# Performance work log

Hardware: AMD Instinct MI355X
Metric: run time of the kernel (lower is better)

## Reference

```python
import jax, jax.numpy as jnp
import numpy as np

B, S, H = 2, 2048, 2048
NH, NKV, D = 32, 8, 64
N_REP = NH // NKV  # 4
THETA = 10000.0


def _rotate_half(x):
    x1, x2 = jnp.split(x, 2, axis=-1)
    return jnp.concatenate([-x2, x1], axis=-1)


def _apply_rope(q, k, position_ids):
    # q: [B,NH,S,D], k: [B,NKV,S,D], position_ids: [B,S]
    inv_freq = 1.0 / (THETA ** (jnp.arange(0, D, 2, dtype=jnp.float32) / D))  # [D/2]
    ang = position_ids[:, None, :, None].astype(jnp.float32) * inv_freq      # [B,1,S,D/2]
    cos = jnp.concatenate([jnp.cos(ang), jnp.cos(ang)], axis=-1)             # [B,1,S,D]
    sin = jnp.concatenate([jnp.sin(ang), jnp.sin(ang)], axis=-1)
    q = q * cos + _rotate_half(q) * sin
    k = k * cos + _rotate_half(k) * sin
    return q, k


def setup_inputs() -> dict:
    key = jax.random.key(0)
    k1, k2, k3, k4 = jax.random.split(key, 4)
    hidden_states = jax.random.normal(k1, (B, S, H), dtype=jnp.float32)
    position_ids = jnp.broadcast_to(jnp.arange(S, dtype=jnp.int64 if jax.config.jax_enable_x64 else jnp.int32)[None, :], (B, S))
    Wq = jax.random.normal(k2, (H, NH * D), dtype=jnp.float32) * 0.02
    Wkv = jax.random.normal(k3, (H, NKV * 2 * D), dtype=jnp.float32) * 0.02
    Wo = jax.random.normal(k4, (H, H), dtype=jnp.float32) * 0.02
    return {"hidden_states": hidden_states, "position_ids": position_ids,
            "Wq": Wq, "Wkv": Wkv, "Wo": Wo}


def reference(hidden_states, position_ids, Wq, Wkv, Wo):
    b, s, _ = hidden_states.shape
    # fused QKV projections (Linear, no bias)
    q = (hidden_states @ Wq).reshape(b, s, NH, D).transpose(0, 2, 1, 3)      # [B,NH,S,D]
    kv = (hidden_states @ Wkv).reshape(b, s, NKV, 2, D)
    k = kv[:, :, :, 0, :].transpose(0, 2, 1, 3)                              # [B,NKV,S,D]
    v = kv[:, :, :, 1, :].transpose(0, 2, 1, 3)                              # [B,NKV,S,D]
    # rotary embedding
    q, k = _apply_rope(q, k, position_ids)
    # GQA: repeat_interleave K/V heads
    k = jnp.repeat(k, N_REP, axis=1)                                         # [B,NH,S,D]
    v = jnp.repeat(v, N_REP, axis=1)
    # causal SDPA (eval mode: dropout_p = 0)
    scale = 1.0 / np.sqrt(D)
    scores = jnp.einsum('bhqd,bhkd->bhqk', q, k) * scale                     # [B,NH,S,S]
    causal = jnp.tril(jnp.ones((s, s), dtype=bool))
    scores = jnp.where(causal[None, None], scores, jnp.finfo(scores.dtype).min)
    probs = jax.nn.softmax(scores, axis=-1)
    ctx = jnp.einsum('bhqk,bhkd->bhqd', probs, v)                            # [B,NH,S,D]
    ctx = ctx.transpose(0, 2, 1, 3).reshape(b, s, H)
    return ctx @ Wo
```

## Files before the change

### kernel.cpp

```cpp
#include <hip/hip_runtime.h>

typedef __bf16 bf16_t;
typedef __bf16 bf16x8 __attribute__((ext_vector_type(8)));
typedef __bf16 bf16x4 __attribute__((ext_vector_type(4)));
typedef float f32x4 __attribute__((ext_vector_type(4)));

#define DEV static __device__ __forceinline__

DEV void gload16(const void* g, void* lds) {
  __builtin_amdgcn_global_load_lds((__attribute__((address_space(1))) void*)g,
                                   (__attribute__((address_space(3))) void*)lds, 16, 0, 0);
}

DEV f32x4 mfma16(bf16x8 a, bf16x8 b, f32x4 c) {
  return __builtin_amdgcn_mfma_f32_16x16x32_bf16(a, b, c, 0, 0, 0);
}

DEV void transpose_blk(const float* __restrict__ in, bf16_t* __restrict__ out,
                       int R, int C, int bx, int by, int tid, float (*tile)[33]) {
  const int tx = tid & 31, ty = tid >> 5;
  const int rb = by * 32, cb = bx * 32;
#pragma unroll
  for (int i = 0; i < 32; i += 8)
    tile[ty + i][tx] = in[(size_t)(rb + ty + i) * C + (cb + tx)];
  __syncthreads();
#pragma unroll
  for (int i = 0; i < 32; i += 8)
    out[(size_t)(cb + ty + i) * R + (rb + tx)] = (bf16_t)tile[tx][ty + i];
}

__global__ __launch_bounds__(256) void k_prep(const float* __restrict__ hs,
                                              bf16_t* __restrict__ Xbf,
                                              const float* __restrict__ Wq,
                                              const float* __restrict__ Wkv,
                                              const float* __restrict__ Wo,
                                              bf16_t* __restrict__ Wqkvt,
                                              bf16_t* __restrict__ Wot,
                                              const int* __restrict__ pos_ids,
                                              float2* __restrict__ tbl) {
  __shared__ float tile[32][33];
  const int bid = blockIdx.x, tid = threadIdx.x;
  if (bid < 8192) {
    const int i = (bid * 256 + tid) * 4;
    float4 v = *(const float4*)(hs + i);
    bf16x4 o;
    o[0] = (bf16_t)v.x; o[1] = (bf16_t)v.y; o[2] = (bf16_t)v.z; o[3] = (bf16_t)v.w;
    *(bf16x4*)(Xbf + i) = o;
  } else if (bid < 8192 + 512) {
    const int token = (bid - 8192) * 8 + (tid >> 5);
    const int d2 = tid & 31;
    const float p = (float)pos_ids[token];
    const float freq = exp2f(-(float)d2 / 32.0f * log2f(10000.0f));
    const float a = p * freq;
    tbl[token * 32 + d2] = make_float2(cosf(a), sinf(a));
  } else if (bid < 8192 + 512 + 4096) {
    const int local = bid - (8192 + 512);
    transpose_blk(Wq, Wqkvt, 2048, 2048, local & 63, local >> 6, tid, tile);
  } else if (bid < 8192 + 512 + 4096 + 2048) {
    const int local = bid - (8192 + 512 + 4096);
    transpose_blk(Wkv, Wqkvt + (size_t)2048 * 2048, 2048, 1024,
                  local & 31, local >> 5, tid, tile);
  } else {
    const int local = bid - (8192 + 512 + 4096 + 2048);
    transpose_blk(Wo, Wot, 2048, 2048, local & 63, local >> 6, tid, tile);
  }
}

#define PH_MID()                                            \
  __builtin_amdgcn_s_barrier();                             \
  asm volatile("s_waitcnt lgkmcnt(0)" ::: "memory");        \
  __builtin_amdgcn_sched_barrier(0);                        \
  __builtin_amdgcn_s_setprio(1)

#define PH_END()                                            \
  __builtin_amdgcn_s_setprio(0);                            \
  __builtin_amdgcn_s_barrier()

#define STAGE_A(bi, st, h)                                                      \
  do {                                                                          \
    const bf16_t* _s = gA + (size_t)(brow + (h) * 128 + r0) * gK + (st) * 64 + l0 * 8; \
    gload16(_s, &As[bi][((h) * 1024 + tid) * 8]);                               \
    gload16(_s + (size_t)64 * gK, &As[bi][((h) * 1024 + 512 + tid) * 8]);       \
  } while (0)

#define STAGE_B(bi, st, h)                                                      \
  do {                                                                          \
    const bf16_t* _s = gB + (size_t)(bcol + (h) * 128 + r0) * gK + (st) * 64 + l0 * 8; \
    gload16(_s, &Bs[bi][((h) * 1024 + tid) * 8]);                               \
    gload16(_s + (size_t)64 * gK, &Bs[bi][((h) * 1024 + 512 + tid) * 8]);       \
  } while (0)

#define QLOADA(dst, bi, mh)                                                     \
  _Pragma("unroll")                                                             \
  for (int mq = 0; mq < 4; ++mq) {                                              \
    const int R = wm * 128 + (mh) * 64 + mq * 16 + c15;                         \
    dst[mq][0] = *(const bf16x8*)(&As[bi][(R * 8 + (g ^ (R & 7))) * 8]);        \
    dst[mq][1] = *(const bf16x8*)(&As[bi][(R * 8 + ((4 + g) ^ (R & 7))) * 8]);  \
  }

#define QLOADB(dst, bi, nh)                                                     \
  _Pragma("unroll")                                                             \
  for (int nq = 0; nq < 2; ++nq) {                                              \
    const int R = wn * 64 + ((nh) * 2 + nq) * 16 + c15;                         \
    dst[nq][0] = *(const bf16x8*)(&Bs[bi][(R * 8 + (g ^ (R & 7))) * 8]);        \
    dst[nq][1] = *(const bf16x8*)(&Bs[bi][(R * 8 + ((4 + g) ^ (R & 7))) * 8]);  \
  }

#define QMFMA(afX, bfX, mh, nh)                                                 \
  _Pragma("unroll")                                                             \
  for (int nq = 0; nq < 2; ++nq)                                                \
    _Pragma("unroll")                                                           \
    for (int mq = 0; mq < 4; ++mq)                                              \
      acc[(mh) * 4 + mq][(nh) * 2 + nq] =                                       \
          mfma16(afX[mq][1], bfX[nq][1],                                        \
                 mfma16(afX[mq][0], bfX[nq][0], acc[(mh) * 4 + mq][(nh) * 2 + nq]));

__global__ __launch_bounds__(512, 2) void k_gemm_qkv(
    const bf16_t* __restrict__ gA, const bf16_t* __restrict__ gB,
    const float2* __restrict__ tbl,
    bf16_t* __restrict__ Qp, bf16_t* __restrict__ Kp, bf16_t* __restrict__ Vt) {
  __shared__ __align__(16) bf16_t As[2][256 * 64];
  __shared__ __align__(16) bf16_t Bs[2][256 * 64];
  const int gK = 2048, NBX = 12;
  const int tid = threadIdx.x;
  const int lane = tid & 63, w = tid >> 6;
  const int c15 = lane & 15, g = lane >> 4;
  const int wm = w >> 2, wn = w & 3;

  const int cpx = (int)gridDim.x >> 3;
  const int u = ((int)blockIdx.x & 7) * cpx + ((int)blockIdx.x >> 3);
  const int bx = u % NBX, by = u / NBX;
  const int brow = by * 256, bcol = bx * 256;

  const int r0 = tid >> 3, p0 = tid & 7;
  const int l0 = p0 ^ (r0 & 7);

  const f32x4 fzero = {0.f, 0.f, 0.f, 0.f};
  f32x4 acc[8][4];
#pragma unroll
  for (int m = 0; m < 8; ++m)
#pragma unroll
    for (int n = 0; n < 4; ++n) acc[m][n] = fzero;

  const int NT = gK >> 6;

  STAGE_A(0, 0, 0); STAGE_A(0, 0, 1); STAGE_B(0, 0, 0); STAGE_B(0, 0, 1);
  STAGE_A(1, 1, 0); STAGE_A(1, 1, 1); STAGE_B(1, 1, 0); STAGE_B(1, 1, 1);
  asm volatile("s_waitcnt vmcnt(8)" ::: "memory");
  __builtin_amdgcn_s_barrier();

  for (int t = 0; t < NT; ++t) {
    const int bi = t & 1;
    const int st2 = (t + 2 < NT) ? t + 2 : NT - 1;
    bf16x8 af0[4][2], af1[4][2], bf0[2][2], bf1[2][2];

    QLOADA(af0, bi, 0);
    QLOADB(bf0, bi, 0);
    PH_MID();
    QMFMA(af0, bf0, 0, 0);
    PH_END();

    QLOADB(bf1, bi, 1);
    PH_MID();
    QMFMA(af0, bf1, 0, 1);
    PH_END();

    QLOADA(af1, bi, 1);
    STAGE_B(bi, st2, 0);
    PH_MID();
    QMFMA(af1, bf1, 1, 1);
    PH_END();

    STAGE_B(bi, st2, 1);
    STAGE_A(bi, st2, 0);
    STAGE_A(bi, st2, 1);
    asm volatile("s_waitcnt vmcnt(8)" ::: "memory");
    PH_MID();
    QMFMA(af1, bf0, 1, 0);
    PH_END();
  }

  const int seg = bcol + wn * 64;
  const int wrow = brow + wm * 128;
  const float QSCALE = 0.125f * 1.44269504088896340736f;
  if (seg < 2048) {
    const int hq = seg >> 6;
#pragma unroll
    for (int m = 0; m < 8; ++m)
#pragma unroll
      for (int r = 0; r < 4; ++r) {
        const int row = wrow + m * 16 + g * 4 + r;
        const int bb = row >> 11, s = row & 2047;
        const float2 cs0 = tbl[row * 32 + c15];
        const float2 cs1 = tbl[row * 32 + 16 + c15];
        bf16_t* dst = Qp + (((size_t)bb * 32 + hq) * 2048 + s) * 64;
        dst[c15]      = (bf16_t)((acc[m][0][r] * cs0.x - acc[m][2][r] * cs0.y) * QSCALE);
        dst[32 + c15] = (bf16_t)((acc[m][2][r] * cs0.x + acc[m][0][r] * cs0.y) * QSCALE);
        dst[16 + c15] = (bf16_t)((acc[m][1][r] * cs1.x - acc[m][3][r] * cs1.y) * QSCALE);
        dst[48 + c15] = (bf16_t)((acc[m][3][r] * cs1.x + acc[m][1][r] * cs1.y) * QSCALE);
      }
  } else {
    const int cc = seg - 2048;
    const int kvh = cc >> 7;
    if (((cc >> 6) & 1) == 0) {
#pragma unroll
      for (int m = 0; m < 8; ++m)
#pragma unroll
        for (int r = 0; r < 4; ++r) {
          const int row = wrow + m * 16 + g * 4 + r;
          const int bb = row >> 11, s = row & 2047;
          const float2 cs0 = tbl[row * 32 + c15];
          const float2 cs1 = tbl[row * 32 + 16 + c15];
          bf16_t* dst = Kp + (((size_t)bb * 8 + kvh) * 2048 + s) * 64;
          dst[c15]      = (bf16_t)(acc[m][0][r] * cs0.x - acc[m][2][r] * cs0.y);
          dst[32 + c15] = (bf16_t)(acc[m][2][r] * cs0.x + acc[m][0][r] * cs0.y);
          dst[16 + c15] = (bf16_t)(acc[m][1][r] * cs1.x - acc[m][3][r] * cs1.y);
          dst[48 + c15] = (bf16_t)(acc[m][3][r] * cs1.x + acc[m][1][r] * cs1.y);
        }
    } else {
#pragma unroll
      for (int m = 0; m < 8; ++m) {
        const int row0 = wrow + m * 16 + g * 4;
        const int bb = row0 >> 11, s0 = row0 & 2047;
#pragma unroll
        for (int n = 0; n < 4; ++n) {
          bf16x4 o;
#pragma unroll
          for (int r = 0; r < 4; ++r) o[r] = (bf16_t)acc[m][n][r];
          const int d = n * 16 + c15;
          *(bf16x4*)(Vt + ((size_t)(bb * 8 + kvh) * 64 + d) * 2048 + s0) = o;
        }
      }
    }
  }
}

#define OSTAGE_A(bi, st, h)                                                     \
  do {                                                                          \
    const bf16_t* _s = gA + (size_t)(brow + (h) * 128 + r0) * gK + (st) * 64 + l0 * 8; \
    gload16(_s, &As[bi][((h) * 1024 + tid) * 8]);                               \
    gload16(_s + (size_t)64 * gK, &As[bi][((h) * 1024 + 512 + tid) * 8]);       \
  } while (0)

#define OSTAGE_B(bi, st)                                                        \
  do {                                                                          \
    const bf16_t* _s = gB + (size_t)(bcol + r0) * gK + (st) * 64 + l0 * 8;      \
    gload16(_s, &Bs[bi][tid * 8]);                                              \
    gload16(_s + (size_t)64 * gK, &Bs[bi][(512 + tid) * 8]);                    \
  } while (0)

#define OLOADA(dst, bi, mh)                                                     \
  _Pragma("unroll")                                                             \
  for (int mq = 0; mq < 4; ++mq) {                                              \
    const int R = wm * 128 + (mh) * 64 + mq * 16 + c15;                         \
    dst[mq][0] = *(const bf16x8*)(&As[bi][(R * 8 + (g ^ (R & 7))) * 8]);        \
    dst[mq][1] = *(const bf16x8*)(&As[bi][(R * 8 + ((4 + g) ^ (R & 7))) * 8]);  \
  }

#define OLOADB(bi)                                                              \
  _Pragma("unroll")                                                             \
  for (int nq = 0; nq < 2; ++nq) {                                              \
    const int R = wn * 32 + nq * 16 + c15;                                      \
    bfr[nq][0] = *(const bf16x8*)(&Bs[bi][(R * 8 + (g ^ (R & 7))) * 8]);        \
    bfr[nq][1] = *(const bf16x8*)(&Bs[bi][(R * 8 + ((4 + g) ^ (R & 7))) * 8]);  \
  }

#define OMFMAQ(afX, mh)                                                         \
  _Pragma("unroll")                                                             \
  for (int nq = 0; nq < 2; ++nq)                                                \
    _Pragma("unroll")                                                           \
    for (int mq = 0; mq < 4; ++mq)                                              \
      acc[(mh) * 4 + mq][nq] =                                                  \
          mfma16(afX[mq][1], bfr[nq][1],                                        \
                 mfma16(afX[mq][0], bfr[nq][0], acc[(mh) * 4 + mq][nq]));

__global__ __launch_bounds__(512, 2) void k_gemm_out(
    const bf16_t* __restrict__ gA, const bf16_t* __restrict__ gB,
    float* __restrict__ C) {
  __shared__ __align__(16) bf16_t As[2][256 * 64];
  __shared__ __align__(16) bf16_t Bs[2][128 * 64];
  const int gK = 2048, NBX = 16, ldc = 2048;
  const int tid = threadIdx.x;
  const int lane = tid & 63, w = tid >> 6;
  const int c15 = lane & 15, g = lane >> 4;
  const int wm = w >> 2, wn = w & 3;

  const int cpx = (int)gridDim.x >> 3;
  const int u = ((int)blockIdx.x & 7) * cpx + ((int)blockIdx.x >> 3);
  const int bx = u % NBX, by = u / NBX;
  const int brow = by * 256, bcol = bx * 128;

  const int r0 = tid >> 3, p0 = tid & 7;
  const int l0 = p0 ^ (r0 & 7);

  const f32x4 fzero = {0.f, 0.f, 0.f, 0.f};
  f32x4 acc[8][2];
#pragma unroll
  for (int m = 0; m < 8; ++m)
#pragma unroll
    for (int n = 0; n < 2; ++n) acc[m][n] = fzero;

  const int NT = gK >> 6;

  OSTAGE_A(0, 0, 0); OSTAGE_A(0, 0, 1); OSTAGE_B(0, 0);
  OSTAGE_A(1, 1, 0); OSTAGE_B(1, 1);
  asm volatile("s_waitcnt vmcnt(4)" ::: "memory");
  __builtin_amdgcn_s_barrier();

  for (int t = 0; t < NT; ++t) {
    const int bi = t & 1, oi = bi ^ 1;
    const int st1 = (t + 1 < NT) ? t + 1 : NT - 1;
    const int st2 = (t + 2 < NT) ? t + 2 : NT - 1;
    bf16x8 af0[4][2], af1[4][2], bfr[2][2];

    OLOADA(af0, bi, 0);
    OLOADB(bi);
    OSTAGE_A(oi, st1, 1);
    PH_MID();
    OMFMAQ(af0, 0);
    PH_END();

    OLOADA(af1, bi, 1);
    OSTAGE_A(bi, st2, 0);
    OSTAGE_B(bi, st2);
    asm volatile("s_waitcnt vmcnt(4)" ::: "memory");
    PH_MID();
    OMFMAQ(af1, 1);
    PH_END();
  }

#pragma unroll
  for (int m = 0; m < 8; ++m)
#pragma unroll
    for (int n = 0; n < 2; ++n)
#pragma unroll
      for (int r = 0; r < 4; ++r) {
        const int row = brow + wm * 128 + m * 16 + g * 4 + r;
        const int col = bcol + wn * 32 + n * 16 + c15;
        C[(size_t)row * ldc + col] = acc[m][n][r];
      }
}

__global__ __launch_bounds__(256, 3) void k_attn(const bf16_t* __restrict__ Qp,
                                                 const bf16_t* __restrict__ Kp,
                                                 const bf16_t* __restrict__ Vt,
                                                 bf16_t* __restrict__ ctx) {
  const int wgid = blockIdx.x;
  const int gidx = wgid & 15;
  const int j    = wgid >> 4;
  const int b = gidx >> 3, kvh = gidx & 7;
  const int qs = 63 - j;
  const int tid = threadIdx.x, lane = tid & 63, w = tid >> 6;
  const int h = kvh * 4 + w;
  const int c15 = lane & 15, g = lane >> 4;

  __shared__ __align__(16) bf16_t Ks[2][64 * 64];
  __shared__ __align__(16) bf16_t Vs[2][64 * 64];
  __shared__ __align__(16) bf16_t Pw[4][32 * 64];
  bf16_t* pw = &Pw[w][0];

  const int q0 = qs * 32;

  bf16x8 aq[2][2];
#pragma unroll
  for (int m = 0; m < 2; ++m) {
    const bf16_t* Qrow = Qp + (((size_t)b * 32 + h) * 2048 + q0 + m * 16 + c15) * 64;
    aq[m][0] = *(const bf16x8*)(Qrow + g * 8);
    aq[m][1] = *(const bf16x8*)(Qrow + 32 + g * 8);
  }
  asm volatile("s_waitcnt vmcnt(0)" ::: "memory");

  const bf16_t* Kb = Kp + ((size_t)b * 8 + kvh) * (size_t)(2048 * 64);
  const bf16_t* Vb = Vt + ((size_t)b * 8 + kvh) * (size_t)(64 * 2048);

  const int c0 = tid,      r0 = c0 >> 3, l0 = (c0 & 7) ^ (r0 & 7);
  const int c1 = tid + 256, r1 = c1 >> 3, l1 = (c1 & 7) ^ (r1 & 7);
  const int dst0 = (w * 64) * 8, dst1 = (w * 64 + 256) * 8;

  const f32x4 fzero = {0.f, 0.f, 0.f, 0.f};
  f32x4 acc[2][4];
  f32x4 lsum[2];
#pragma unroll
  for (int m = 0; m < 2; ++m) {
    lsum[m] = fzero;
#pragma unroll
    for (int n = 0; n < 4; ++n) acc[m][n] = fzero;
  }
  bf16x8 bones;
#pragma unroll
  for (int j2 = 0; j2 < 8; ++j2) bones[j2] = (bf16_t)1.0f;

  const int ntw = qs / 2 + 1;

  gload16(Kb + (size_t)r0 * 64 + l0 * 8, &Ks[0][dst0]);
  gload16(Kb + (size_t)r1 * 64 + l1 * 8, &Ks[0][dst1]);
  gload16(Vb + (size_t)r0 * 2048 + l0 * 8, &Vs[0][dst0]);
  gload16(Vb + (size_t)r1 * 2048 + l1 * 8, &Vs[0][dst1]);

  for (int t = 0; t < ntw; ++t) {
    const int kvbase = t * 64;
    const int tnb = (t + 1 < ntw ? t + 1 : t) * 64;
    const int nb = (t + 1) & 1, cb = t & 1;

    gload16(Kb + (size_t)(tnb + r0) * 64 + l0 * 8, &Ks[nb][dst0]);
    gload16(Kb + (size_t)(tnb + r1) * 64 + l1 * 8, &Ks[nb][dst1]);
    gload16(Vb + (size_t)r0 * 2048 + tnb + l0 * 8, &Vs[nb][dst0]);
    gload16(Vb + (size_t)r1 * 2048 + tnb + l1 * 8, &Vs[nb][dst1]);
    asm volatile("s_waitcnt vmcnt(4)" ::: "memory");
    __builtin_amdgcn_s_barrier();

    const bf16_t* Kc = &Ks[cb][0];
    f32x4 sv[2][4];
    __builtin_amdgcn_s_setprio(1);
#pragma unroll
    for (int n = 0; n < 4; ++n) {
      const int row = n * 16 + c15;
      const bf16x8 bk0 = *(const bf16x8*)(Kc + row * 64 + ((g ^ (row & 7)) << 3));
      const bf16x8 bk1 = *(const bf16x8*)(Kc + row * 64 + (((4 + g) ^ (row & 7)) << 3));
      sv[0][n] = mfma16(aq[0][1], bk1, mfma16(aq[0][0], bk0, fzero));
      sv[1][n] = mfma16(aq[1][1], bk1, mfma16(aq[1][0], bk0, fzero));
    }
    __builtin_amdgcn_s_setprio(0);

    if (kvbase + 63 > q0) {
#pragma unroll
      for (int n = 0; n < 4; ++n)
#pragma unroll
        for (int r = 0; r < 4; ++r) {
          const int col = kvbase + n * 16 + c15;
          if (col > q0 + g * 4 + r)      sv[0][n][r] = -1e30f;
          if (col > q0 + 16 + g * 4 + r) sv[1][n][r] = -1e30f;
        }
    }
#pragma unroll
    for (int n = 0; n < 4; ++n)
#pragma unroll
      for (int r = 0; r < 4; ++r) {
        const int col = n * 16 + c15;
        const int rp0 = g * 4 + r, rp1 = 16 + g * 4 + r;
        pw[rp0 * 64 + ((((col >> 3) ^ (rp0 & 7)) << 3) | (col & 7))] = (bf16_t)exp2f(sv[0][n][r]);
        pw[rp1 * 64 + ((((col >> 3) ^ (rp1 & 7)) << 3) | (col & 7))] = (bf16_t)exp2f(sv[1][n][r]);
      }
    asm volatile("s_waitcnt lgkmcnt(0)" ::: "memory");
    __builtin_amdgcn_sched_barrier(0);

    bf16x8 ap[2][2];
#pragma unroll
    for (int m = 0; m < 2; ++m) {
      const int q = m * 16 + c15;
      ap[m][0] = *(const bf16x8*)(pw + q * 64 + ((g ^ (q & 7)) << 3));
      ap[m][1] = *(const bf16x8*)(pw + q * 64 + (((4 + g) ^ (q & 7)) << 3));
    }
    const bf16_t* Vc = &Vs[cb][0];
    __builtin_amdgcn_s_setprio(1);
#pragma unroll
    for (int m = 0; m < 2; ++m)
      lsum[m] = mfma16(ap[m][1], bones, mfma16(ap[m][0], bones, lsum[m]));
#pragma unroll
    for (int n = 0; n < 4; ++n) {
      const int row = n * 16 + c15;
      const bf16x8 bv0 = *(const bf16x8*)(Vc + row * 64 + ((g ^ (row & 7)) << 3));
      const bf16x8 bv1 = *(const bf16x8*)(Vc + row * 64 + (((4 + g) ^ (row & 7)) << 3));
#pragma unroll
      for (int m = 0; m < 2; ++m)
        acc[m][n] = mfma16(ap[m][1], bv1, mfma16(ap[m][0], bv0, acc[m][n]));
    }
    __builtin_amdgcn_s_setprio(0);
    __builtin_amdgcn_s_barrier();
  }

#pragma unroll
  for (int m = 0; m < 2; ++m) {
    float inv[4];
#pragma unroll
    for (int r = 0; r < 4; ++r) inv[r] = 1.0f / lsum[m][r];
#pragma unroll
    for (int n = 0; n < 4; ++n)
#pragma unroll
      for (int r = 0; r < 4; ++r) {
        const int rowq = q0 + m * 16 + g * 4 + r;
        const int col = h * 64 + n * 16 + c15;
        ctx[((size_t)b * 2048 + rowq) * 2048 + col] = (bf16_t)(acc[m][n][r] * inv[r]);
      }
  }
}

extern "C" void kernel_launch(void* const* d_in, const int* in_sizes, int n_in,
                              void* d_out, int out_size, void* d_ws, size_t ws_size,
                              hipStream_t stream) {
  const float* hs  = (const float*)d_in[0];
  const int*   pos = (const int*)d_in[1];
  const float* Wq  = (const float*)d_in[2];
  const float* Wkv = (const float*)d_in[3];
  const float* Wo  = (const float*)d_in[4];
  float* out = (float*)d_out;
  (void)in_sizes; (void)n_in; (void)out_size; (void)ws_size;

  char* p = (char*)d_ws;
  bf16_t* Xbf   = (bf16_t*)p; p += (size_t)4096 * 2048 * 2;
  bf16_t* Wqkvt = (bf16_t*)p; p += (size_t)3072 * 2048 * 2;
  bf16_t* Wot   = (bf16_t*)p; p += (size_t)2048 * 2048 * 2;
  float2* tbl   = (float2*)p; p += (size_t)4096 * 32 * 8;
  bf16_t* Qp    = (bf16_t*)p; p += (size_t)2 * 32 * 2048 * 64 * 2;
  bf16_t* Kp    = (bf16_t*)p; p += (size_t)2 * 8 * 2048 * 64 * 2;
  bf16_t* Vt    = (bf16_t*)p; p += (size_t)2 * 8 * 64 * 2048 * 2;
  bf16_t* ctx   = (bf16_t*)p; p += (size_t)4096 * 2048 * 2;

  k_prep<<<18944, 256, 0, stream>>>(hs, Xbf, Wq, Wkv, Wo, Wqkvt, Wot, pos, tbl);
  k_gemm_qkv<<<192, 512, 0, stream>>>(Xbf, Wqkvt, tbl, Qp, Kp, Vt);
  k_attn<<<1024, 256, 0, stream>>>(Qp, Kp, Vt, ctx);
  k_gemm_out<<<256, 512, 0, stream>>>(ctx, Wot, out);
}
```

Baseline: 190.0 us.

## Retile QKV GEMM to 256x192 for full-CU grid and stage epilogue through LDS

The QKV projection GEMM changes from 256x256 tiles (192 blocks) to 256x192 tiles (256 blocks), so the grid matches the 256 CUs of the MI355X and no CUs sit idle in a partial wave. The main loop is restructured into two MFMA phases per K-step, with A and B staging for the next tiles interleaved in new places. The epilogue now writes accumulators to LDS and has each thread write whole 64-wide rows with RoPE applied, using vectorized Q/K stores. The trade-off is extra LDS traffic and barriers in the epilogue, scalar strided V-transpose stores, and lower MFMA reuse per B load.

```diff
diff --git a/kernel.cpp b/kernel.cpp
--- a/kernel.cpp
+++ b/kernel.cpp
@@ -76,52 +76,54 @@
   __builtin_amdgcn_s_setprio(0);                            \
   __builtin_amdgcn_s_barrier()
 
-#define STAGE_A(bi, st, h)                                                      \
+#define QSTAGE_A(bi, st, h)                                                     \
   do {                                                                          \
-    const bf16_t* _s = gA + (size_t)(brow + (h) * 128 + r0) * gK + (st) * 64 + l0 * 8; \
-    gload16(_s, &As[bi][((h) * 1024 + tid) * 8]);                               \
-    gload16(_s + (size_t)64 * gK, &As[bi][((h) * 1024 + 512 + tid) * 8]);       \
+    const bf16_t* _s = gA + (size_t)(brow + (h) * 128 + r0) * 2048 + (st) * 64 + l0 * 8; \
+    gload16(_s, SMEM + (bi) * 16384 + ((h) * 1024 + tid) * 8);                  \
+    gload16(_s + (size_t)64 * 2048, SMEM + (bi) * 16384 + ((h) * 1024 + 512 + tid) * 8); \
   } while (0)
 
-#define STAGE_B(bi, st, h)                                                      \
+#define QSTAGE_B(bi, st)                                                        \
   do {                                                                          \
-    const bf16_t* _s = gB + (size_t)(bcol + (h) * 128 + r0) * gK + (st) * 64 + l0 * 8; \
-    gload16(_s, &Bs[bi][((h) * 1024 + tid) * 8]);                               \
-    gload16(_s + (size_t)64 * gK, &Bs[bi][((h) * 1024 + 512 + tid) * 8]);       \
+    const bf16_t* _s = gB + (size_t)(bcol + r0) * 2048 + (st) * 64 + l0 * 8;    \
+    bf16_t* _d = SMEM + 32768 + (bi) * 12288;                                   \
+    gload16(_s, _d + tid * 8);                                                  \
+    gload16(_s + (size_t)64 * 2048, _d + (512 + tid) * 8);                      \
+    gload16(_s + (size_t)128 * 2048, _d + (1024 + tid) * 8);                    \
   } while (0)
 
 #define QLOADA(dst, bi, mh)                                                     \
   _Pragma("unroll")                                                             \
   for (int mq = 0; mq < 4; ++mq) {                                              \
     const int R = wm * 128 + (mh) * 64 + mq * 16 + c15;                         \
-    dst[mq][0] = *(const bf16x8*)(&As[bi][(R * 8 + (g ^ (R & 7))) * 8]);        \
-    dst[mq][1] = *(const bf16x8*)(&As[bi][(R * 8 + ((4 + g) ^ (R & 7))) * 8]);  \
-  }
-
-#define QLOADB(dst, bi, nh)                                                     \
+    const bf16_t* _a = SMEM + (bi) * 16384;                                     \
+    dst[mq][0] = *(const bf16x8*)(_a + (R * 8 + (g ^ (R & 7))) * 8);            \
+    dst[mq][1] = *(const bf16x8*)(_a + (R * 8 + ((4 + g) ^ (R & 7))) * 8);      \
+  }
+
+#define QLOADB(bi)                                                              \
   _Pragma("unroll")                                                             \
-  for (int nq = 0; nq < 2; ++nq) {                                              \
-    const int R = wn * 64 + ((nh) * 2 + nq) * 16 + c15;                         \
-    dst[nq][0] = *(const bf16x8*)(&Bs[bi][(R * 8 + (g ^ (R & 7))) * 8]);        \
-    dst[nq][1] = *(const bf16x8*)(&Bs[bi][(R * 8 + ((4 + g) ^ (R & 7))) * 8]);  \
-  }
-
-#define QMFMA(afX, bfX, mh, nh)                                                 \
+  for (int nq = 0; nq < 3; ++nq) {                                              \
+    const int R = wn * 48 + nq * 16 + c15;                                      \
+    const bf16_t* _b = SMEM + 32768 + (bi) * 12288;                             \
+    bfr[nq][0] = *(const bf16x8*)(_b + (R * 8 + (g ^ (R & 7))) * 8);            \
+    bfr[nq][1] = *(const bf16x8*)(_b + (R * 8 + ((4 + g) ^ (R & 7))) * 8);      \
+  }
+
+#define QMFMA(afX, mh)                                                          \
   _Pragma("unroll")                                                             \
-  for (int nq = 0; nq < 2; ++nq)                                                \
+  for (int nq = 0; nq < 3; ++nq)                                                \
     _Pragma("unroll")                                                           \
     for (int mq = 0; mq < 4; ++mq)                                              \
-      acc[(mh) * 4 + mq][(nh) * 2 + nq] =                                       \
-          mfma16(afX[mq][1], bfX[nq][1],                                        \
-                 mfma16(afX[mq][0], bfX[nq][0], acc[(mh) * 4 + mq][(nh) * 2 + nq]));
+      acc[(mh) * 4 + mq][nq] =                                                  \
+          mfma16(afX[mq][1], bfr[nq][1],                                        \
+                 mfma16(afX[mq][0], bfr[nq][0], acc[(mh) * 4 + mq][nq]));
 
 __global__ __launch_bounds__(512, 2) void k_gemm_qkv(
     const bf16_t* __restrict__ gA, const bf16_t* __restrict__ gB,
     const float2* __restrict__ tbl,
     bf16_t* __restrict__ Qp, bf16_t* __restrict__ Kp, bf16_t* __restrict__ Vt) {
-  __shared__ __align__(16) bf16_t As[2][256 * 64];
-  __shared__ __align__(16) bf16_t Bs[2][256 * 64];
-  const int gK = 2048, NBX = 12;
+  __shared__ __align__(16) bf16_t SMEM[2 * 16384 + 2 * 12288];
   const int tid = threadIdx.x;
   const int lane = tid & 63, w = tid >> 6;
   const int c15 = lane & 15, g = lane >> 4;
@@ -129,106 +131,106 @@
 
   const int cpx = (int)gridDim.x >> 3;
   const int u = ((int)blockIdx.x & 7) * cpx + ((int)blockIdx.x >> 3);
-  const int bx = u % NBX, by = u / NBX;
-  const int brow = by * 256, bcol = bx * 256;
+  const int bx = u & 15, by = u >> 4;
+  const int brow = by * 256, bcol = bx * 192;
 
   const int r0 = tid >> 3, p0 = tid & 7;
   const int l0 = p0 ^ (r0 & 7);
 
   const f32x4 fzero = {0.f, 0.f, 0.f, 0.f};
-  f32x4 acc[8][4];
+  f32x4 acc[8][3];
 #pragma unroll
   for (int m = 0; m < 8; ++m)
 #pragma unroll
-    for (int n = 0; n < 4; ++n) acc[m][n] = fzero;
-
-  const int NT = gK >> 6;
-
-  STAGE_A(0, 0, 0); STAGE_A(0, 0, 1); STAGE_B(0, 0, 0); STAGE_B(0, 0, 1);
-  STAGE_A(1, 1, 0); STAGE_A(1, 1, 1); STAGE_B(1, 1, 0); STAGE_B(1, 1, 1);
-  asm volatile("s_waitcnt vmcnt(8)" ::: "memory");
+    for (int n = 0; n < 3; ++n) acc[m][n] = fzero;
+
+  const int NT = 2048 >> 6;
+
+  QSTAGE_A(0, 0, 0); QSTAGE_A(0, 0, 1); QSTAGE_B(0, 0);
+  QSTAGE_A(1, 1, 0); QSTAGE_B(1, 1);
+  asm volatile("s_waitcnt vmcnt(5)" ::: "memory");
   __builtin_amdgcn_s_barrier();
 
   for (int t = 0; t < NT; ++t) {
-    const int bi = t & 1;
+    const int bi = t & 1, oi = bi ^ 1;
+    const int st1 = (t + 1 < NT) ? t + 1 : NT - 1;
     const int st2 = (t + 2 < NT) ? t + 2 : NT - 1;
-    bf16x8 af0[4][2], af1[4][2], bf0[2][2], bf1[2][2];
+    bf16x8 af0[4][2], af1[4][2], bfr[3][2];
 
     QLOADA(af0, bi, 0);
-    QLOADB(bf0, bi, 0);
+    QLOADB(bi);
+    QSTAGE_A(oi, st1, 1);
     PH_MID();
-    QMFMA(af0, bf0, 0, 0);
+    QMFMA(af0, 0);
     PH_END();
 
-    QLOADB(bf1, bi, 1);
+    QLOADA(af1, bi, 1);
+    QSTAGE_A(bi, st2, 0);
+    QSTAGE_B(bi, st2);
+    asm volatile("s_waitcnt vmcnt(5)" ::: "memory");
     PH_MID();
-    QMFMA(af0, bf1, 0, 1);
+    QMFMA(af1, 1);
     PH_END();
-
-    QLOADA(af1, bi, 1);
-    STAGE_B(bi, st2, 0);
-    PH_MID();
-    QMFMA(af1, bf1, 1, 1);
-    PH_END();
-
-    STAGE_B(bi, st2, 1);
-    STAGE_A(bi, st2, 0);
-    STAGE_A(bi, st2, 1);
-    asm volatile("s_waitcnt vmcnt(8)" ::: "memory");
-    PH_MID();
-    QMFMA(af1, bf0, 1, 0);
-    PH_END();
-  }
-
-  const int seg = bcol + wn * 64;
-  const int wrow = brow + wm * 128;
+  }
+
+  float* ex = (float*)SMEM;
   const float QSCALE = 0.125f * 1.44269504088896340736f;
-  if (seg < 2048) {
-    const int hq = seg >> 6;
-#pragma unroll
-    for (int m = 0; m < 8; ++m)
-#pragma unroll
-      for (int r = 0; r < 4; ++r) {
-        const int row = wrow + m * 16 + g * 4 + r;
-        const int bb = row >> 11, s = row & 2047;
-        const float2 cs0 = tbl[row * 32 + c15];
-        const float2 cs1 = tbl[row * 32 + 16 + c15];
+#pragma unroll 1
+  for (int eh = 0; eh < 2; ++eh) {
+    __syncthreads();
+#pragma unroll
+    for (int mm = 0; mm < 4; ++mm) {
+      const int m = eh * 4 + mm;
+#pragma unroll
+      for (int n = 0; n < 3; ++n)
+#pragma unroll
+        for (int r = 0; r < 4; ++r) {
+          const int lr = wm * 64 + mm * 16 + g * 4 + r;
+          ex[lr * 193 + wn * 48 + n * 16 + c15] = acc[m][n][r];
+        }
+    }
+    __syncthreads();
+    if (tid < 384) {
+      const int lr = tid & 127, hh = tid >> 7;
+      const int grow = brow + (lr >> 6) * 128 + eh * 64 + (lr & 63);
+      const int bb = grow >> 11, s = grow & 2047;
+      const int gcol = bcol + hh * 64;
+      const float* exr = ex + lr * 193 + hh * 64;
+      if (gcol < 2048) {
+        const int hq = gcol >> 6;
+        bf16_t o[64];
+#pragma unroll
+        for (int d2 = 0; d2 < 32; ++d2) {
+          const float2 cs = tbl[grow * 32 + d2];
+          const float v1 = exr[d2], v2 = exr[32 + d2];
+          o[d2]      = (bf16_t)((v1 * cs.x - v2 * cs.y) * QSCALE);
+          o[32 + d2] = (bf16_t)((v2 * cs.x + v1 * cs.y) * QSCALE);
+        }
         bf16_t* dst = Qp + (((size_t)bb * 32 + hq) * 2048 + s) * 64;
-        dst[c15]      = (bf16_t)((acc[m][0][r] * cs0.x - acc[m][2][r] * cs0.y) * QSCALE);
-        dst[32 + c15] = (bf16_t)((acc[m][2][r] * cs0.x + acc[m][0][r] * cs0.y) * QSCALE);
-        dst[16 + c15] = (bf16_t)((acc[m][1][r] * cs1.x - acc[m][3][r] * cs1.y) * QSCALE);
-        dst[48 + c15] = (bf16_t)((acc[m][3][r] * cs1.x + acc[m][1][r] * cs1.y) * QSCALE);
-      }
-  } else {
-    const int cc = seg - 2048;
-    const int kvh = cc >> 7;
-    if (((cc >> 6) & 1) == 0) {
-#pragma unroll
-      for (int m = 0; m < 8; ++m)
-#pragma unroll
-        for (int r = 0; r < 4; ++r) {
-          const int row = wrow + m * 16 + g * 4 + r;
-          const int bb = row >> 11, s = row & 2047;
-          const float2 cs0 = tbl[row * 32 + c15];
-          const float2 cs1 = tbl[row * 32 + 16 + c15];
+#pragma unroll
+        for (int j = 0; j < 8; ++j)
+          *(bf16x8*)(dst + j * 8) = *(bf16x8*)(o + j * 8);
+      } else {
+        const int cc = gcol - 2048;
+        const int kvh = cc >> 7;
+        if (((cc >> 6) & 1) == 0) {
+          bf16_t o[64];
+#pragma unroll
+          for (int d2 = 0; d2 < 32; ++d2) {
+            const float2 cs = tbl[grow * 32 + d2];
+            const float v1 = exr[d2], v2 = exr[32 + d2];
+            o[d2]      = (bf16_t)(v1 * cs.x - v2 * cs.y);
+            o[32 + d2] = (bf16_t)(v2 * cs.x + v1 * cs.y);
+          }
           bf16_t* dst = Kp + (((size_t)bb * 8 + kvh) * 2048 + s) * 64;
-          dst[c15]      = (bf16_t)(acc[m][0][r] * cs0.x - acc[m][2][r] * cs0.y);
-          dst[32 + c15] = (bf16_t)(acc[m][2][r] * cs0.x + acc[m][0][r] * cs0.y);
-          dst[16 + c15] = (bf16_t)(acc[m][1][r] * cs1.x - acc[m][3][r] * cs1.y);
-          dst[48 + c15] = (bf16_t)(acc[m][3][r] * cs1.x + acc[m][1][r] * cs1.y);
-        }
-    } else {
-#pragma unroll
-      for (int m = 0; m < 8; ++m) {
-        const int row0 = wrow + m * 16 + g * 4;
-        const int bb = row0 >> 11, s0 = row0 & 2047;
-#pragma unroll
-        for (int n = 0; n < 4; ++n) {
-          bf16x4 o;
-#pragma unroll
-          for (int r = 0; r < 4; ++r) o[r] = (bf16_t)acc[m][n][r];
-          const int d = n * 16 + c15;
-          *(bf16x4*)(Vt + ((size_t)(bb * 8 + kvh) * 64 + d) * 2048 + s0) = o;
+#pragma unroll
+          for (int j = 0; j < 8; ++j)
+            *(bf16x8*)(dst + j * 8) = *(bf16x8*)(o + j * 8);
+        } else {
+          bf16_t* dst = Vt + (size_t)(bb * 8 + kvh) * 64 * 2048 + s;
+#pragma unroll
+          for (int d = 0; d < 64; ++d)
+            dst[(size_t)d * 2048] = (bf16_t)exr[d];
         }
       }
     }
@@ -507,7 +509,7 @@
   bf16_t* ctx   = (bf16_t*)p; p += (size_t)4096 * 2048 * 2;
 
   k_prep<<<18944, 256, 0, stream>>>(hs, Xbf, Wq, Wkv, Wo, Wqkvt, Wot, pos, tbl);
-  k_gemm_qkv<<<192, 512, 0, stream>>>(Xbf, Wqkvt, tbl, Qp, Kp, Vt);
+  k_gemm_qkv<<<256, 512, 0, stream>>>(Xbf, Wqkvt, tbl, Qp, Kp, Vt);
   k_attn<<<1024, 256, 0, stream>>>(Qp, Kp, Vt, ctx);
   k_gemm_out<<<256, 512, 0, stream>>>(ctx, Wot, out);
 }
```

After: 210.8 us. 10.9% more time.
